# Optimization experiments

Hardware: AMD Instinct MI355X
Metric: run time of the kernel (lower is better)

The kernel has to match this reference:

```python
import jax, jax.numpy as jnp
import numpy as np

N_NODES = 100000
N_EDGES = 500000
HID = 128


def setup_inputs() -> dict:
    key = jax.random.key(0)
    k = jax.random.split(key, 8)
    h = jax.random.normal(k[0], (N_NODES, HID), dtype=jnp.float32)
    src = jax.random.randint(k[1], (N_EDGES,), 0, N_NODES)
    dst = jax.random.randint(k[2], (N_EDGES,), 0, N_NODES)
    # torch nn.Linear weights are [out, in]
    W1 = jax.random.normal(k[3], (HID, 2 * HID), dtype=jnp.float32) * (1.0 / np.sqrt(2 * HID))
    b1 = jnp.zeros((HID,), dtype=jnp.float32)
    W2 = jax.random.normal(k[4], (1, HID), dtype=jnp.float32) * (1.0 / np.sqrt(HID))
    b2 = jnp.zeros((1,), dtype=jnp.float32)
    W3 = jax.random.normal(k[5], (1, 1), dtype=jnp.float32)
    b3 = jnp.zeros((1,), dtype=jnp.float32)
    return {"h": h, "src": src, "dst": dst, "W1": W1, "b1": b1, "W2": W2, "b2": b2, "W3": W3, "b3": b3}


def reference(h, src, dst, W1, b1, W2, b2, W3, b3):
    # gather src/dst node features per edge and concat -> [E, 2*HID]
    x = jnp.concatenate([h[src], h[dst]], axis=1)
    x = jax.nn.relu(x @ W1.T + b1)            # [E, HID]
    x = jax.nn.relu(x @ W2.T + b2)            # [E, 1]
    x = jax.nn.relu(x @ W3.T + b3)            # [E, 1]
    return jax.nn.sigmoid(x)                  # [E, 1]
```

## Files before the change

kernel.cpp:

```cpp
#include <hip/hip_runtime.h>
#include <hip/hip_bf16.h>


#define HID 128

using short8 = __attribute__((ext_vector_type(8))) short;
using f32x4  = __attribute__((ext_vector_type(4))) float;

typedef unsigned int uint32;

static __device__ __forceinline__ unsigned short f2bf(float f) {
    uint32 u = __float_as_uint(f);
    u += 0x7fffu + ((u >> 16) & 1u);
    return (unsigned short)(u >> 16);
}
static __device__ __forceinline__ uint32 pk2(float a, float b) {
    return ((uint32)f2bf(a)) | (((uint32)f2bf(b)) << 16);
}
static __device__ __forceinline__ float bflo(uint32 u) { return __uint_as_float(u << 16); }
static __device__ __forceinline__ float bfhi(uint32 u) { return __uint_as_float(u & 0xffff0000u); }

__global__ __launch_bounds__(256) void prep_kernel(
    const float* __restrict__ W1,
    const float* __restrict__ b1,
    unsigned short* __restrict__ wtab,
    float* __restrict__ bias256)
{
    const int idx  = blockIdx.x * 256 + threadIdx.x;
    const int widx = idx >> 6;
    const int lane = idx & 63;
    const int wave = widx >> 4;
    const int ot   = (widx >> 2) & 3;
    const int ks   = widx & 3;
    const int o    = wave * 64 + ot * 16 + (lane & 15);
    const int row  = o & 127;
    const int col  = ((o >= 128) ? 128 : 0) + ks * 32 + (lane >> 4) * 8;
    const float* p = W1 + row * 256 + col;
    float4 f0 = *(const float4*)p;
    float4 f1 = *(const float4*)(p + 4);
    uint4 st;
    st.x = pk2(f0.x, f0.y);
    st.y = pk2(f0.z, f0.w);
    st.z = pk2(f1.x, f1.y);
    st.w = pk2(f1.z, f1.w);
    *(uint4*)(wtab + (size_t)idx * 8) = st;

    if (idx < 256) bias256[idx] = (idx < 128) ? b1[idx] : 0.0f;
}

#define NT_PER_BLOCK 4

__global__ __launch_bounds__(256) void node_stage_v2_kernel(
    const float* __restrict__ h,
    const unsigned short* __restrict__ wtab,
    const float* __restrict__ bias256,
    unsigned short* __restrict__ AB,
    int N)
{
    __shared__ unsigned short hs[2][16 * 256];

    const int t    = threadIdx.x;
    const int lane = t & 63;
    const int wave = t >> 6;
    const int c    = lane & 15;
    const int q    = lane >> 4;

    short8 vfrag[4][4];
    float4 bias[4];
#pragma unroll
    for (int ot = 0; ot < 4; ++ot) {
#pragma unroll
        for (int ks = 0; ks < 4; ++ks) {
            int widx = (wave * 4 + ot) * 4 + ks;
            vfrag[ot][ks] = *(const short8*)(wtab + ((size_t)widx * 64 + lane) * 8);
        }
        bias[ot] = *(const float4*)(bias256 + wave * 64 + ot * 16 + q * 4);
    }

    const int sr = t >> 4;
    const int sj = t & 15;
    const int ntiles = N >> 4;
    const int nt0 = blockIdx.x * NT_PER_BLOCK;
    if (nt0 >= ntiles) return;

    {
        const float* p = h + (size_t)(nt0 * 16 + sr) * HID + sj * 8;
        float4 f0 = *(const float4*)p;
        float4 f1 = *(const float4*)(p + 4);
        uint4 st;
        st.x = pk2(f0.x, f0.y);
        st.y = pk2(f0.z, f0.w);
        st.z = pk2(f1.x, f1.y);
        st.w = pk2(f1.z, f1.w);
        *(uint4*)(hs[0] + sr * 256 + ((sj ^ sr) * 8)) = st;
    }

#pragma unroll
    for (int it = 0; it < NT_PER_BLOCK; ++it) {
        const int tile = nt0 + it;
        if (tile >= ntiles) break;
        __syncthreads();

        const bool have_next = (it + 1 < NT_PER_BLOCK) && (tile + 1 < ntiles);
        float4 g0, g1;
        if (have_next) {
            const float* p = h + (size_t)((tile + 1) * 16 + sr) * HID + sj * 8;
            g0 = *(const float4*)p;
            g1 = *(const float4*)(p + 4);
        }

        short8 hfrag[4];
#pragma unroll
        for (int ks = 0; ks < 4; ++ks) {
            int blk = (ks * 4 + q) ^ c;
            hfrag[ks] = *(const short8*)(hs[it & 1] + c * 256 + blk * 8);
        }

        f32x4 acc[4];
#pragma unroll
        for (int ot = 0; ot < 4; ++ot) acc[ot] = (f32x4){0.f, 0.f, 0.f, 0.f};

#pragma unroll
        for (int ks = 0; ks < 4; ++ks)
#pragma unroll
            for (int ot = 0; ot < 4; ++ot)
                acc[ot] = __builtin_amdgcn_mfma_f32_16x16x32_bf16(
                    vfrag[ot][ks], hfrag[ks], acc[ot], 0, 0, 0);

        const int node = tile * 16 + c;
#pragma unroll
        for (int ot = 0; ot < 4; ++ot) {
            int o_base = wave * 64 + ot * 16 + q * 4;
            uint2 st;
            st.x = pk2(acc[ot][0] + bias[ot].x, acc[ot][1] + bias[ot].y);
            st.y = pk2(acc[ot][2] + bias[ot].z, acc[ot][3] + bias[ot].w);
            *(uint2*)(AB + (size_t)node * 256 + o_base) = st;
        }

        if (have_next) {
            uint4 st;
            st.x = pk2(g0.x, g0.y);
            st.y = pk2(g0.z, g0.w);
            st.z = pk2(g1.x, g1.y);
            st.w = pk2(g1.z, g1.w);
            *(uint4*)(hs[(it + 1) & 1] + sr * 256 + ((sj ^ sr) * 8)) = st;
        }
    }
}

__global__ __launch_bounds__(256) void node_stage_kernel(
    const float* __restrict__ h,
    const float* __restrict__ W1,
    const float* __restrict__ b1,
    unsigned short* __restrict__ AB,
    int N)
{
    __shared__ unsigned short hs[2][16 * 256];

    const int t    = threadIdx.x;
    const int lane = t & 63;
    const int wave = t >> 6;
    const int c    = lane & 15;
    const int q    = lane >> 4;

    short8 vfrag[4][4];
    float  bias[4][4];
#pragma unroll
    for (int ot = 0; ot < 4; ++ot) {
#pragma unroll
        for (int ks = 0; ks < 4; ++ks) {
            int o   = wave * 64 + ot * 16 + c;
            int row = o & 127;
            int col = ((o >= 128) ? 128 : 0) + ks * 32 + q * 8;
            const float* p = W1 + row * 256 + col;
            float4 f0 = *(const float4*)p;
            float4 f1 = *(const float4*)(p + 4);
            short8 v;
            v[0] = (short)f2bf(f0.x); v[1] = (short)f2bf(f0.y);
            v[2] = (short)f2bf(f0.z); v[3] = (short)f2bf(f0.w);
            v[4] = (short)f2bf(f1.x); v[5] = (short)f2bf(f1.y);
            v[6] = (short)f2bf(f1.z); v[7] = (short)f2bf(f1.w);
            vfrag[ot][ks] = v;
        }
#pragma unroll
        for (int r = 0; r < 4; ++r) {
            int o = wave * 64 + ot * 16 + q * 4 + r;
            bias[ot][r] = (o < 128) ? b1[o] : 0.0f;
        }
    }

    const int sr = t >> 4;
    const int sj = t & 15;
    const int ntiles = N >> 4;
    const int nt0 = blockIdx.x * NT_PER_BLOCK;
    if (nt0 >= ntiles) return;

    {
        const float* p = h + (size_t)(nt0 * 16 + sr) * HID + sj * 8;
        float4 f0 = *(const float4*)p;
        float4 f1 = *(const float4*)(p + 4);
        uint4 st;
        st.x = pk2(f0.x, f0.y);
        st.y = pk2(f0.z, f0.w);
        st.z = pk2(f1.x, f1.y);
        st.w = pk2(f1.z, f1.w);
        *(uint4*)(hs[0] + sr * 256 + ((sj ^ sr) * 8)) = st;
    }

#pragma unroll
    for (int it = 0; it < NT_PER_BLOCK; ++it) {
        const int tile = nt0 + it;
        if (tile >= ntiles) break;
        __syncthreads();

        const bool have_next = (it + 1 < NT_PER_BLOCK) && (tile + 1 < ntiles);
        float4 g0, g1;
        if (have_next) {
            const float* p = h + (size_t)((tile + 1) * 16 + sr) * HID + sj * 8;
            g0 = *(const float4*)p;
            g1 = *(const float4*)(p + 4);
        }

        short8 hfrag[4];
#pragma unroll
        for (int ks = 0; ks < 4; ++ks) {
            int blk = (ks * 4 + q) ^ c;
            hfrag[ks] = *(const short8*)(hs[it & 1] + c * 256 + blk * 8);
        }

        f32x4 acc[4];
#pragma unroll
        for (int ot = 0; ot < 4; ++ot) acc[ot] = (f32x4){0.f, 0.f, 0.f, 0.f};

#pragma unroll
        for (int ks = 0; ks < 4; ++ks)
#pragma unroll
            for (int ot = 0; ot < 4; ++ot)
                acc[ot] = __builtin_amdgcn_mfma_f32_16x16x32_bf16(
                    vfrag[ot][ks], hfrag[ks], acc[ot], 0, 0, 0);

        const int node = tile * 16 + c;
#pragma unroll
        for (int ot = 0; ot < 4; ++ot) {
            int o_base = wave * 64 + ot * 16 + q * 4;
            uint2 st;
            st.x = pk2(acc[ot][0] + bias[ot][0], acc[ot][1] + bias[ot][1]);
            st.y = pk2(acc[ot][2] + bias[ot][2], acc[ot][3] + bias[ot][3]);
            *(uint2*)(AB + (size_t)node * 256 + o_base) = st;
        }

        if (have_next) {
            uint4 st;
            st.x = pk2(g0.x, g0.y);
            st.y = pk2(g0.z, g0.w);
            st.z = pk2(g1.x, g1.y);
            st.w = pk2(g1.z, g1.w);
            *(uint4*)(hs[(it + 1) & 1] + sr * 256 + ((sj ^ sr) * 8)) = st;
        }
    }
}

__global__ __launch_bounds__(256) void edge_stage_kernel(
    const unsigned short* __restrict__ AB,
    const int* __restrict__ src,
    const int* __restrict__ dst,
    const float* __restrict__ W2,
    const float* __restrict__ b2,
    const float* __restrict__ W3,
    const float* __restrict__ b3,
    float* __restrict__ out,
    int E)
{
    const int lane = threadIdx.x & 63;
    const int wave = threadIdx.x >> 6;
    const int sub  = lane & 15;
    const int eg   = lane >> 4;
    const int e    = blockIdx.x * 16 + wave * 4 + eg;
    if (e >= E) return;

    const int s = src[e];
    const int d = dst[e];

    const uint4 ua = *(const uint4*)(AB + (size_t)s * 256 + sub * 8);
    const uint4 ub = *(const uint4*)(AB + (size_t)d * 256 + 128 + sub * 8);
    const float4 w0 = *(const float4*)(W2 + sub * 8);
    const float4 w1 = *(const float4*)(W2 + sub * 8 + 4);

    float p;
    {
        float t0 = fmaxf(bflo(ua.x) + bflo(ub.x), 0.0f);
        float t1 = fmaxf(bfhi(ua.x) + bfhi(ub.x), 0.0f);
        float t2 = fmaxf(bflo(ua.y) + bflo(ub.y), 0.0f);
        float t3 = fmaxf(bfhi(ua.y) + bfhi(ub.y), 0.0f);
        float t4 = fmaxf(bflo(ua.z) + bflo(ub.z), 0.0f);
        float t5 = fmaxf(bfhi(ua.z) + bfhi(ub.z), 0.0f);
        float t6 = fmaxf(bflo(ua.w) + bflo(ub.w), 0.0f);
        float t7 = fmaxf(bfhi(ua.w) + bfhi(ub.w), 0.0f);
        p  = t0 * w0.x;
        p  = fmaf(t1, w0.y, p);
        p  = fmaf(t2, w0.z, p);
        p  = fmaf(t3, w0.w, p);
        p  = fmaf(t4, w1.x, p);
        p  = fmaf(t5, w1.y, p);
        p  = fmaf(t6, w1.z, p);
        p  = fmaf(t7, w1.w, p);
    }

#pragma unroll
    for (int m = 8; m >= 1; m >>= 1) p += __shfl_xor(p, m, 64);

    if (sub == 0) {
        float y2 = fmaxf(p + b2[0], 0.0f);
        float y3 = fmaxf(W3[0] * y2 + b3[0], 0.0f);
        out[e] = 1.0f / (1.0f + __expf(-y3));
    }
}

__global__ __launch_bounds__(256) void edge_direct_kernel(
    const float* __restrict__ h,
    const int* __restrict__ src,
    const int* __restrict__ dst,
    const float* __restrict__ W1,
    const float* __restrict__ b1,
    const float* __restrict__ W2,
    const float* __restrict__ b2,
    const float* __restrict__ W3,
    const float* __restrict__ b3,
    float* __restrict__ out,
    int E)
{
    __shared__ float x[256];
    __shared__ float red[4];
    const int e = blockIdx.x;
    if (e >= E) return;
    const int t = threadIdx.x;
    const int s = src[e];
    const int d = dst[e];

    if (t < 128) x[t] = h[(size_t)s * HID + t];
    else         x[t] = h[(size_t)d * HID + (t - 128)];
    __syncthreads();

    float contrib = 0.0f;
    if (t < 128) {
        float acc = b1[t];
        const float* wr = W1 + t * 256;
        for (int k = 0; k < 256; ++k) acc = fmaf(wr[k], x[k], acc);
        contrib = fmaxf(acc, 0.0f) * W2[t];
    }
#pragma unroll
    for (int m = 32; m >= 1; m >>= 1) contrib += __shfl_xor(contrib, m, 64);
    if ((t & 63) == 0) red[t >> 6] = contrib;
    __syncthreads();
    if (t == 0) {
        float p = red[0] + red[1] + red[2] + red[3];
        float y2 = fmaxf(p + b2[0], 0.0f);
        float y3 = fmaxf(W3[0] * y2 + b3[0], 0.0f);
        out[e] = 1.0f / (1.0f + __expf(-y3));
    }
}

extern "C" void kernel_launch(void* const* d_in, const int* in_sizes, int n_in,
                              void* d_out, int out_size, void* d_ws, size_t ws_size,
                              hipStream_t stream) {
    const float* h   = (const float*)d_in[0];
    const int*   src = (const int*)d_in[1];
    const int*   dst = (const int*)d_in[2];
    const float* W1  = (const float*)d_in[3];
    const float* b1  = (const float*)d_in[4];
    const float* W2  = (const float*)d_in[5];
    const float* b2  = (const float*)d_in[6];
    const float* W3  = (const float*)d_in[7];
    const float* b3  = (const float*)d_in[8];
    float* out = (float*)d_out;

    const int N = in_sizes[0] / HID;
    const int E = in_sizes[1];

    const size_t ab_bytes  = (size_t)N * 256 * sizeof(unsigned short);
    const size_t wtab_off  = (ab_bytes + 255) & ~(size_t)255;
    const size_t wtab_bytes = (size_t)64 * 64 * 8 * sizeof(unsigned short);
    const size_t bias_off  = wtab_off + wtab_bytes;
    const size_t need_v2   = bias_off + 256 * sizeof(float);

    const int node_tiles = (N + 15) / 16;
    const int nblocks = (node_tiles + NT_PER_BLOCK - 1) / NT_PER_BLOCK;

    if (need_v2 <= ws_size) {
        unsigned short* AB   = (unsigned short*)d_ws;
        unsigned short* wtab = (unsigned short*)((char*)d_ws + wtab_off);
        float* bias256       = (float*)((char*)d_ws + bias_off);
        prep_kernel<<<16, 256, 0, stream>>>(W1, b1, wtab, bias256);
        node_stage_v2_kernel<<<nblocks, 256, 0, stream>>>(h, wtab, bias256, AB, N);
        edge_stage_kernel<<<(E + 15) / 16, 256, 0, stream>>>(AB, src, dst, W2, b2, W3, b3, out, E);
    } else if (ab_bytes <= ws_size) {
        unsigned short* AB = (unsigned short*)d_ws;
        node_stage_kernel<<<nblocks, 256, 0, stream>>>(h, W1, b1, AB, N);
        edge_stage_kernel<<<(E + 15) / 16, 256, 0, stream>>>(AB, src, dst, W2, b2, W3, b3, out, E);
    } else {
        edge_direct_kernel<<<E, 256, 0, stream>>>(h, src, dst, W1, b1, W2, b2, W3, b3, out, E);
    }
}
```

Measured before the change: 152.3 us.

## Process 64-node tiles per block in node stage and widen per-lane edge loads

The node-stage kernel now loads a 64-node tile of h into shared memory in one pass, using a new XOR swizzle, and runs a 4x4 grid of MFMA accumulators per wave. This replaces the earlier double-buffered loop over 16-node tiles and reuses each weight fragment across four node tiles with a single barrier. The edge kernel now gives each edge 8 lanes instead of 16, each loading 32 bytes per side, which halves the shuffle reduction and doubles edges per block. The fallback node kernel becomes a grid-stride loop without prefetch. The cost is more accumulator registers in the node kernel and fewer lanes per gather in the edge kernel.

```diff
diff --git a/kernel.cpp b/kernel.cpp
--- a/kernel.cpp
+++ b/kernel.cpp
@@ -48,16 +48,14 @@
     if (idx < 256) bias256[idx] = (idx < 128) ? b1[idx] : 0.0f;
 }
 
-#define NT_PER_BLOCK 4
-
-__global__ __launch_bounds__(256) void node_stage_v2_kernel(
+__global__ __launch_bounds__(256) void node_stage_v3_kernel(
     const float* __restrict__ h,
     const unsigned short* __restrict__ wtab,
     const float* __restrict__ bias256,
     unsigned short* __restrict__ AB,
     int N)
 {
-    __shared__ unsigned short hs[2][16 * 256];
+    __shared__ unsigned short hs[64 * 128];
 
     const int t    = threadIdx.x;
     const int lane = t & 63;
@@ -77,73 +75,64 @@
         bias[ot] = *(const float4*)(bias256 + wave * 64 + ot * 16 + q * 4);
     }
 
-    const int sr = t >> 4;
-    const int sj = t & 15;
-    const int ntiles = N >> 4;
-    const int nt0 = blockIdx.x * NT_PER_BLOCK;
-    if (nt0 >= ntiles) return;
-
-    {
-        const float* p = h + (size_t)(nt0 * 16 + sr) * HID + sj * 8;
-        float4 f0 = *(const float4*)p;
-        float4 f1 = *(const float4*)(p + 4);
-        uint4 st;
-        st.x = pk2(f0.x, f0.y);
-        st.y = pk2(f0.z, f0.w);
-        st.z = pk2(f1.x, f1.y);
-        st.w = pk2(f1.z, f1.w);
-        *(uint4*)(hs[0] + sr * 256 + ((sj ^ sr) * 8)) = st;
-    }
-
-#pragma unroll
-    for (int it = 0; it < NT_PER_BLOCK; ++it) {
-        const int tile = nt0 + it;
-        if (tile >= ntiles) break;
-        __syncthreads();
-
-        const bool have_next = (it + 1 < NT_PER_BLOCK) && (tile + 1 < ntiles);
-        float4 g0, g1;
-        if (have_next) {
-            const float* p = h + (size_t)((tile + 1) * 16 + sr) * HID + sj * 8;
-            g0 = *(const float4*)p;
-            g1 = *(const float4*)(p + 4);
-        }
-
+    const int n0 = blockIdx.x * 64;
+
+    float4 g[8];
+#pragma unroll
+    for (int j = 0; j < 8; ++j) {
+        int e4 = j * 256 + t;
+        int rl = e4 >> 5;
+        int grow = n0 + rl;
+        if (grow >= N) grow = N - 1;
+        g[j] = *(const float4*)(h + (size_t)grow * HID + (e4 & 31) * 4);
+    }
+#pragma unroll
+    for (int j = 0; j < 8; ++j) {
+        int e4 = j * 256 + t;
+        int rl = e4 >> 5;
+        int u  = e4 & 31;
+        uint2 w2;
+        w2.x = pk2(g[j].x, g[j].y);
+        w2.y = pk2(g[j].z, g[j].w);
+        *(uint2*)(hs + rl * 128 + ((u ^ ((rl & 15) << 1)) << 2)) = w2;
+    }
+    __syncthreads();
+
+    f32x4 acc[4][4];
+#pragma unroll
+    for (int nt = 0; nt < 4; ++nt)
+#pragma unroll
+        for (int ot = 0; ot < 4; ++ot) acc[nt][ot] = (f32x4){0.f, 0.f, 0.f, 0.f};
+
+#pragma unroll
+    for (int ks = 0; ks < 4; ++ks) {
         short8 hfrag[4];
 #pragma unroll
-        for (int ks = 0; ks < 4; ++ks) {
-            int blk = (ks * 4 + q) ^ c;
-            hfrag[ks] = *(const short8*)(hs[it & 1] + c * 256 + blk * 8);
-        }
-
-        f32x4 acc[4];
-#pragma unroll
-        for (int ot = 0; ot < 4; ++ot) acc[ot] = (f32x4){0.f, 0.f, 0.f, 0.f};
-
-#pragma unroll
-        for (int ks = 0; ks < 4; ++ks)
+        for (int nt = 0; nt < 4; ++nt) {
+            int r  = nt * 16 + c;
+            int u0 = ks * 8 + q * 2;
+            hfrag[nt] = *(const short8*)(hs + r * 128 + ((u0 ^ (c << 1)) << 2));
+        }
+#pragma unroll
+        for (int nt = 0; nt < 4; ++nt)
 #pragma unroll
             for (int ot = 0; ot < 4; ++ot)
-                acc[ot] = __builtin_amdgcn_mfma_f32_16x16x32_bf16(
-                    vfrag[ot][ks], hfrag[ks], acc[ot], 0, 0, 0);
-
-        const int node = tile * 16 + c;
-#pragma unroll
-        for (int ot = 0; ot < 4; ++ot) {
-            int o_base = wave * 64 + ot * 16 + q * 4;
-            uint2 st;
-            st.x = pk2(acc[ot][0] + bias[ot].x, acc[ot][1] + bias[ot].y);
-            st.y = pk2(acc[ot][2] + bias[ot].z, acc[ot][3] + bias[ot].w);
-            *(uint2*)(AB + (size_t)node * 256 + o_base) = st;
-        }
-
-        if (have_next) {
-            uint4 st;
-            st.x = pk2(g0.x, g0.y);
-            st.y = pk2(g0.z, g0.w);
-            st.z = pk2(g1.x, g1.y);
-            st.w = pk2(g1.z, g1.w);
-            *(uint4*)(hs[(it + 1) & 1] + sr * 256 + ((sj ^ sr) * 8)) = st;
+                acc[nt][ot] = __builtin_amdgcn_mfma_f32_16x16x32_bf16(
+                    vfrag[ot][ks], hfrag[nt], acc[nt][ot], 0, 0, 0);
+    }
+
+#pragma unroll
+    for (int nt = 0; nt < 4; ++nt) {
+        const int node = n0 + nt * 16 + c;
+        if (node < N) {
+#pragma unroll
+            for (int ot = 0; ot < 4; ++ot) {
+                int o_base = wave * 64 + ot * 16 + q * 4;
+                uint2 st;
+                st.x = pk2(acc[nt][ot][0] + bias[ot].x, acc[nt][ot][1] + bias[ot].y);
+                st.y = pk2(acc[nt][ot][2] + bias[ot].z, acc[nt][ot][3] + bias[ot].w);
+                *(uint2*)(AB + (size_t)node * 256 + o_base) = st;
+            }
         }
     }
 }
@@ -155,7 +144,7 @@
     unsigned short* __restrict__ AB,
     int N)
 {
-    __shared__ unsigned short hs[2][16 * 256];
+    __shared__ unsigned short hsb[16 * 256];
 
     const int t    = threadIdx.x;
     const int lane = t & 63;
@@ -192,46 +181,31 @@
     const int sr = t >> 4;
     const int sj = t & 15;
     const int ntiles = N >> 4;
-    const int nt0 = blockIdx.x * NT_PER_BLOCK;
-    if (nt0 >= ntiles) return;
-
-    {
-        const float* p = h + (size_t)(nt0 * 16 + sr) * HID + sj * 8;
-        float4 f0 = *(const float4*)p;
-        float4 f1 = *(const float4*)(p + 4);
-        uint4 st;
-        st.x = pk2(f0.x, f0.y);
-        st.y = pk2(f0.z, f0.w);
-        st.z = pk2(f1.x, f1.y);
-        st.w = pk2(f1.z, f1.w);
-        *(uint4*)(hs[0] + sr * 256 + ((sj ^ sr) * 8)) = st;
-    }
-
-#pragma unroll
-    for (int it = 0; it < NT_PER_BLOCK; ++it) {
-        const int tile = nt0 + it;
-        if (tile >= ntiles) break;
+    for (int tile = blockIdx.x; tile < ntiles; tile += gridDim.x) {
+        int n0 = tile * 16;
+        {
+            const float* p = h + (size_t)(n0 + sr) * HID + sj * 8;
+            float4 f0 = *(const float4*)p;
+            float4 f1 = *(const float4*)(p + 4);
+            uint4 st;
+            st.x = pk2(f0.x, f0.y);
+            st.y = pk2(f0.z, f0.w);
+            st.z = pk2(f1.x, f1.y);
+            st.w = pk2(f1.z, f1.w);
+            *(uint4*)(hsb + sr * 256 + ((sj ^ sr) * 8)) = st;
+        }
         __syncthreads();
-
-        const bool have_next = (it + 1 < NT_PER_BLOCK) && (tile + 1 < ntiles);
-        float4 g0, g1;
-        if (have_next) {
-            const float* p = h + (size_t)((tile + 1) * 16 + sr) * HID + sj * 8;
-            g0 = *(const float4*)p;
-            g1 = *(const float4*)(p + 4);
-        }
 
         short8 hfrag[4];
 #pragma unroll
         for (int ks = 0; ks < 4; ++ks) {
             int blk = (ks * 4 + q) ^ c;
-            hfrag[ks] = *(const short8*)(hs[it & 1] + c * 256 + blk * 8);
+            hfrag[ks] = *(const short8*)(hsb + c * 256 + blk * 8);
         }
 
         f32x4 acc[4];
 #pragma unroll
         for (int ot = 0; ot < 4; ++ot) acc[ot] = (f32x4){0.f, 0.f, 0.f, 0.f};
-
 #pragma unroll
         for (int ks = 0; ks < 4; ++ks)
 #pragma unroll
@@ -239,7 +213,7 @@
                 acc[ot] = __builtin_amdgcn_mfma_f32_16x16x32_bf16(
                     vfrag[ot][ks], hfrag[ks], acc[ot], 0, 0, 0);
 
-        const int node = tile * 16 + c;
+        const int node = n0 + c;
 #pragma unroll
         for (int ot = 0; ot < 4; ++ot) {
             int o_base = wave * 64 + ot * 16 + q * 4;
@@ -248,15 +222,7 @@
             st.y = pk2(acc[ot][2] + bias[ot][2], acc[ot][3] + bias[ot][3]);
             *(uint2*)(AB + (size_t)node * 256 + o_base) = st;
         }
-
-        if (have_next) {
-            uint4 st;
-            st.x = pk2(g0.x, g0.y);
-            st.y = pk2(g0.z, g0.w);
-            st.z = pk2(g1.x, g1.y);
-            st.w = pk2(g1.z, g1.w);
-            *(uint4*)(hs[(it + 1) & 1] + sr * 256 + ((sj ^ sr) * 8)) = st;
-        }
+        __syncthreads();
     }
 }
 
@@ -273,41 +239,64 @@
 {
     const int lane = threadIdx.x & 63;
     const int wave = threadIdx.x >> 6;
-    const int sub  = lane & 15;
-    const int eg   = lane >> 4;
-    const int e    = blockIdx.x * 16 + wave * 4 + eg;
+    const int sub  = lane & 7;
+    const int eg   = lane >> 3;
+    const int e    = blockIdx.x * 32 + wave * 8 + eg;
     if (e >= E) return;
 
     const int s = src[e];
     const int d = dst[e];
 
-    const uint4 ua = *(const uint4*)(AB + (size_t)s * 256 + sub * 8);
-    const uint4 ub = *(const uint4*)(AB + (size_t)d * 256 + 128 + sub * 8);
-    const float4 w0 = *(const float4*)(W2 + sub * 8);
-    const float4 w1 = *(const float4*)(W2 + sub * 8 + 4);
+    const unsigned short* pa = AB + (size_t)s * 256 + sub * 16;
+    const unsigned short* pb = AB + (size_t)d * 256 + 128 + sub * 16;
+    const uint4 ua0 = *(const uint4*)pa;
+    const uint4 ua1 = *(const uint4*)(pa + 8);
+    const uint4 ub0 = *(const uint4*)pb;
+    const uint4 ub1 = *(const uint4*)(pb + 8);
+
+    const float4 w0 = *(const float4*)(W2 + sub * 16);
+    const float4 w1 = *(const float4*)(W2 + sub * 16 + 4);
+    const float4 w2v = *(const float4*)(W2 + sub * 16 + 8);
+    const float4 w3v = *(const float4*)(W2 + sub * 16 + 12);
 
     float p;
     {
-        float t0 = fmaxf(bflo(ua.x) + bflo(ub.x), 0.0f);
-        float t1 = fmaxf(bfhi(ua.x) + bfhi(ub.x), 0.0f);
-        float t2 = fmaxf(bflo(ua.y) + bflo(ub.y), 0.0f);
-        float t3 = fmaxf(bfhi(ua.y) + bfhi(ub.y), 0.0f);
-        float t4 = fmaxf(bflo(ua.z) + bflo(ub.z), 0.0f);
-        float t5 = fmaxf(bfhi(ua.z) + bfhi(ub.z), 0.0f);
-        float t6 = fmaxf(bflo(ua.w) + bflo(ub.w), 0.0f);
-        float t7 = fmaxf(bfhi(ua.w) + bfhi(ub.w), 0.0f);
-        p  = t0 * w0.x;
-        p  = fmaf(t1, w0.y, p);
-        p  = fmaf(t2, w0.z, p);
-        p  = fmaf(t3, w0.w, p);
-        p  = fmaf(t4, w1.x, p);
-        p  = fmaf(t5, w1.y, p);
-        p  = fmaf(t6, w1.z, p);
-        p  = fmaf(t7, w1.w, p);
-    }
-
-#pragma unroll
-    for (int m = 8; m >= 1; m >>= 1) p += __shfl_xor(p, m, 64);
+        float t0 = fmaxf(bflo(ua0.x) + bflo(ub0.x), 0.0f);
+        float t1 = fmaxf(bfhi(ua0.x) + bfhi(ub0.x), 0.0f);
+        float t2 = fmaxf(bflo(ua0.y) + bflo(ub0.y), 0.0f);
+        float t3 = fmaxf(bfhi(ua0.y) + bfhi(ub0.y), 0.0f);
+        float t4 = fmaxf(bflo(ua0.z) + bflo(ub0.z), 0.0f);
+        float t5 = fmaxf(bfhi(ua0.z) + bfhi(ub0.z), 0.0f);
+        float t6 = fmaxf(bflo(ua0.w) + bflo(ub0.w), 0.0f);
+        float t7 = fmaxf(bfhi(ua0.w) + bfhi(ub0.w), 0.0f);
+        p = t0 * w0.x;
+        p = fmaf(t1, w0.y, p);
+        p = fmaf(t2, w0.z, p);
+        p = fmaf(t3, w0.w, p);
+        p = fmaf(t4, w1.x, p);
+        p = fmaf(t5, w1.y, p);
+        p = fmaf(t6, w1.z, p);
+        p = fmaf(t7, w1.w, p);
+        float s0 = fmaxf(bflo(ua1.x) + bflo(ub1.x), 0.0f);
+        float s1 = fmaxf(bfhi(ua1.x) + bfhi(ub1.x), 0.0f);
+        float s2 = fmaxf(bflo(ua1.y) + bflo(ub1.y), 0.0f);
+        float s3 = fmaxf(bfhi(ua1.y) + bfhi(ub1.y), 0.0f);
+        float s4 = fmaxf(bflo(ua1.z) + bflo(ub1.z), 0.0f);
+        float s5 = fmaxf(bfhi(ua1.z) + bfhi(ub1.z), 0.0f);
+        float s6 = fmaxf(bflo(ua1.w) + bflo(ub1.w), 0.0f);
+        float s7 = fmaxf(bfhi(ua1.w) + bfhi(ub1.w), 0.0f);
+        p = fmaf(s0, w2v.x, p);
+        p = fmaf(s1, w2v.y, p);
+        p = fmaf(s2, w2v.z, p);
+        p = fmaf(s3, w2v.w, p);
+        p = fmaf(s4, w3v.x, p);
+        p = fmaf(s5, w3v.y, p);
+        p = fmaf(s6, w3v.z, p);
+        p = fmaf(s7, w3v.w, p);
+    }
+
+#pragma unroll
+    for (int m = 4; m >= 1; m >>= 1) p += __shfl_xor(p, m, 64);
 
     if (sub == 0) {
         float y2 = fmaxf(p + b2[0], 0.0f);
@@ -377,26 +366,24 @@
     const int N = in_sizes[0] / HID;
     const int E = in_sizes[1];
 
-    const size_t ab_bytes  = (size_t)N * 256 * sizeof(unsigned short);
-    const size_t wtab_off  = (ab_bytes + 255) & ~(size_t)255;
+    const size_t ab_bytes   = (size_t)N * 256 * sizeof(unsigned short);
+    const size_t wtab_off   = (ab_bytes + 255) & ~(size_t)255;
     const size_t wtab_bytes = (size_t)64 * 64 * 8 * sizeof(unsigned short);
-    const size_t bias_off  = wtab_off + wtab_bytes;
-    const size_t need_v2   = bias_off + 256 * sizeof(float);
-
-    const int node_tiles = (N + 15) / 16;
-    const int nblocks = (node_tiles + NT_PER_BLOCK - 1) / NT_PER_BLOCK;
+    const size_t bias_off   = wtab_off + wtab_bytes;
+    const size_t need_v2    = bias_off + 256 * sizeof(float);
 
     if (need_v2 <= ws_size) {
         unsigned short* AB   = (unsigned short*)d_ws;
         unsigned short* wtab = (unsigned short*)((char*)d_ws + wtab_off);
         float* bias256       = (float*)((char*)d_ws + bias_off);
         prep_kernel<<<16, 256, 0, stream>>>(W1, b1, wtab, bias256);
-        node_stage_v2_kernel<<<nblocks, 256, 0, stream>>>(h, wtab, bias256, AB, N);
-        edge_stage_kernel<<<(E + 15) / 16, 256, 0, stream>>>(AB, src, dst, W2, b2, W3, b3, out, E);
+        const int nblocks = (N + 63) / 64;
+        node_stage_v3_kernel<<<nblocks, 256, 0, stream>>>(h, wtab, bias256, AB, N);
+        edge_stage_kernel<<<(E + 31) / 32, 256, 0, stream>>>(AB, src, dst, W2, b2, W3, b3, out, E);
     } else if (ab_bytes <= ws_size) {
         unsigned short* AB = (unsigned short*)d_ws;
-        node_stage_kernel<<<nblocks, 256, 0, stream>>>(h, W1, b1, AB, N);
-        edge_stage_kernel<<<(E + 15) / 16, 256, 0, stream>>>(AB, src, dst, W2, b2, W3, b3, out, E);
+        node_stage_kernel<<<1563, 256, 0, stream>>>(h, W1, b1, AB, N);
+        edge_stage_kernel<<<(E + 31) / 32, 256, 0, stream>>>(AB, src, dst, W2, b2, W3, b3, out, E);
     } else {
         edge_direct_kernel<<<E, 256, 0, stream>>>(h, src, dst, W1, b1, W2, b2, W3, b3, out, E);
     }
```

After: 154.3 us. About the same (+1.3%).
